# Performance work log

Hardware: AMD Instinct MI355X
Metric: run time of the kernel (lower is better)

The kernel has to match this reference:

```python
import jax, jax.numpy as jnp
import numpy as np

LP = 512   # paragraph length (sequential steps)
LQ = 512   # question/context length attended over
B = 24     # batch_size global in source
IN = 150   # in_size (encoder output dim)
H = 150    # self.hidden_size = 2*75


def setup_inputs() -> dict:
    key = jax.random.key(0)
    ks = jax.random.split(key, 12)
    sc = 1.0 / np.sqrt(2 * IN)  # keep pre-activations in a sane range
    return {
        "up": jax.random.normal(ks[0], (LP, B, IN), jnp.float32),
        "uq": jax.random.normal(ks[1], (LQ, B, IN), jnp.float32),
        "v0": jax.random.normal(ks[2], (B, H), jnp.float32),
        "V": jax.random.normal(ks[3], (B, H, 1), jnp.float32),
        "Wp": jax.random.normal(ks[4], (H, 2 * IN), jnp.float32) * sc,
        "Wq": jax.random.normal(ks[5], (H, 2 * IN), jnp.float32) * sc,
        "Wv": jax.random.normal(ks[6], (H, H), jnp.float32) * sc,
        "Wg": jax.random.normal(ks[7], (4 * IN, 4 * IN), jnp.float32) * sc,
        "w_ih": jax.random.normal(ks[8], (3 * H, 2 * IN), jnp.float32) * sc,
        "w_hh": jax.random.normal(ks[9], (3 * H, H), jnp.float32) * sc,
        "b_ih": jnp.zeros((3 * H,), jnp.float32),
        "b_hh": jnp.zeros((3 * H,), jnp.float32),
    }


def _gru_cell(x, h, w_ih, w_hh, b_ih, b_hh):
    # torch.nn.GRUCell semantics
    gi = x @ w_ih.T + b_ih            # [B, 3H]
    gh = h @ w_hh.T + b_hh            # [B, 3H]
    i_r, i_z, i_n = jnp.split(gi, 3, axis=1)
    h_r, h_z, h_n = jnp.split(gh, 3, axis=1)
    r = jax.nn.sigmoid(i_r + h_r)
    z = jax.nn.sigmoid(i_z + h_z)
    n = jnp.tanh(i_n + r * h_n)
    return (1.0 - z) * n + z * h


def reference(up, uq, v0, V, Wp, Wq, Wv, Wg, w_ih, w_hh, b_ih, b_hh):
    in_size = up.shape[-1]
    # mixer = arange -> up[mixer] == up, so concat duplicates features
    Up = jnp.concatenate([up, up], axis=-1)   # [lp, B, 2*in]
    Uq = jnp.concatenate([uq, uq], axis=-1)   # [lq, B, 2*in]
    WUq = jnp.einsum('lbd,hd->lbh', Uq, Wq)   # loop-invariant Wq(Uq), [lq,B,H]
    Uq_b = Uq.transpose(1, 0, 2)              # [B, lq, 2*in]
    Vv = V[:, :, 0]                            # [B, H]

    def step(v, Up_i):                         # Up_i: [B, 2*in]
        Wup = Up_i @ Wp.T                      # [B, H]
        Wvv = v @ Wv.T                         # [B, H]
        x = jnp.tanh(WUq + Wup[None] + Wvv[None])      # [lq, B, H]
        s = jnp.einsum('lbh,bh->bl', x, Vv)            # [B, lq]
        a = jax.nn.softmax(s, axis=1)                  # [B, lq]
        c = jnp.einsum('bl,bld->bd', a, Uq_b)          # [B, 2*in]
        r = jnp.concatenate([Up_i, c], axis=1)         # [B, 4*in]
        g = jax.nn.sigmoid(r @ Wg.T)                   # [B, 4*in]
        c_ = (g * r)[:, 2 * in_size:]                  # gated attended vector
        v_new = _gru_cell(c_, v, w_ih, w_hh, b_ih, b_hh)
        return v_new, v_new

    _, vs = jax.lax.scan(step, v0, Up)  # [lp, B, H]
    # nn.Dropout in eval mode = identity
    return vs
```

## Files before the change

### kernel.cpp

```cpp
#include <hip/hip_runtime.h>
#include <hip/hip_fp16.h>

typedef _Float16 h2 __attribute__((ext_vector_type(2)));

#define OFF_EW     0u
#define OFF_UQT    983040u
#define OFF_WAV    1904640u
#define OFF_WGC    1952640u
#define OFF_WIH    1976640u
#define OFF_WQST   2048640u
#define OFF_WPC    2071140u
#define OFF_WGU    2093940u
#define OFF_UPA    2139540u
#define OFF_GU     3982740u
#define OFF_FLAG   7669140u
#define WS_FLOATS  7669156u

__device__ __forceinline__ float fast_rcp(float x) { return __builtin_amdgcn_rcpf(x); }
__device__ __forceinline__ float fast_tanh(float x) {
  return 1.f - 2.f * fast_rcp(__expf(2.f * x) + 1.f);
}
__device__ __forceinline__ float fast_sigmoid(float x) {
  return fast_rcp(1.f + __expf(-x));
}

#if defined(__has_builtin)
#if __has_builtin(__builtin_amdgcn_fdot2)
#define HAVE_FDOT2 1
#endif
#if __has_builtin(__builtin_amdgcn_s_setprio)
#define HAVE_SETPRIO 1
#endif
#endif

__device__ __forceinline__ float fdot2(h2 a, h2 b, float c) {
#ifdef HAVE_FDOT2
  return __builtin_amdgcn_fdot2(a, b, c, false);
#else
  return c + (float)a[0] * (float)b[0] + (float)a[1] * (float)b[1];
#endif
}

__global__ void prep_weights(const float* __restrict__ Wq, const float* __restrict__ Wp,
                             const float* __restrict__ Wv, const float* __restrict__ Wg,
                             const float* __restrict__ w_ih, const float* __restrict__ w_hh,
                             float* __restrict__ ws) {
  float* wqsT = ws + OFF_WQST;
  float* WPC  = ws + OFF_WPC;
  float* WGU  = ws + OFF_WGU;
  _Float16* WAV = (_Float16*)(ws + OFF_WAV);
  _Float16* WGC = (_Float16*)(ws + OFF_WGC);
  _Float16* WIHh = (_Float16*)(ws + OFF_WIH);

  int idx = blockIdx.x * blockDim.x + threadIdx.x;
  int n = gridDim.x * blockDim.x;

  for (int i = idx; i < 150 * 150; i += n) {
    int d = i / 150, h = i - d * 150;
    wqsT[i] = Wq[h * 300 + d] + Wq[h * 300 + d + 150];
  }
  for (int i = idx; i < 600 * 160; i += n) {
    int r = i / 160, h = i - r * 160;
    float v = 0.f;
    if (h < 150) v = (r < 150) ? 2.f * Wv[r * 150 + h] : w_hh[(r - 150) * 150 + h];
    WAV[i] = (_Float16)v;
  }
  for (int i = idx; i < 300 * 160; i += n) {
    int r = i / 160, h = i - r * 160;
    int row = (300 + r) * 600;
    float v = (h < 150) ? Wg[row + 300 + h] + Wg[row + 450 + h] : 0.f;
    WGC[i] = (_Float16)v;
  }
  for (int i = idx; i < 450 * 320; i += n) {
    int r = i / 320, p = i - r * 320;
    float v = (p < 300) ? w_ih[r * 300 + p] : 0.f;
    WIHh[i] = (_Float16)v;
  }
  for (int i = idx; i < 150 * 152; i += n) {
    int h = i / 152, d = i - h * 152;
    WPC[i] = (d < 150) ? 2.f * (Wp[h * 300 + d] + Wp[h * 300 + 150 + d]) : 0.f;
  }
  for (int i = idx; i < 300 * 152; i += n) {
    int r = i / 152, d = i - r * 152;
    int row = (300 + r) * 600;
    WGU[i] = (d < 150) ? Wg[row + d] + Wg[row + 150 + d] : 0.f;
  }
}

__global__ __launch_bounds__(192) void prep_ew(const float* __restrict__ uq, float* __restrict__ ws) {
  const float* wqsT = ws + OFF_WQST;
  _Float16* EW = (_Float16*)(ws + OFF_EW);
  const int l = blockIdx.x, b = blockIdx.y;
  __shared__ float sx[150], sDot[150];
  const int t = threadIdx.x;
  if (t < 150) sx[t] = uq[((size_t)l * 24 + b) * 150 + t];
  __syncthreads();
  if (t < 150) {
    float acc = 0.f;
    for (int d = 0; d < 150; ++d) acc += sx[d] * wqsT[d * 150 + t];
    sDot[t] = acc;
  }
  __syncthreads();
  if (t < 160) {
    float val = 1.f;
    if (t < 150) {
      val = __expf(2.f * sDot[t]);
      val = fminf(fmaxf(val, 1e-7f), 60000.f);
    }
    EW[((size_t)b * 512 + l) * 160 + t] = (_Float16)val;
  }
}

__global__ void prep_uqt(const float* __restrict__ uq, float* __restrict__ ws) {
  _Float16* UQT = (_Float16*)(ws + OFF_UQT);
  int idx = blockIdx.x * blockDim.x + threadIdx.x;
  int n = gridDim.x * blockDim.x;
  for (int m = idx; m < 24 * 150 * 512; m += n) {
    int b = m / (150 * 512);
    int rem = m - b * 150 * 512;
    int r = rem >> 9;
    int l = rem & 511;
    UQT[m] = (_Float16)uq[((size_t)l * 24 + b) * 150 + r];
  }
}

__global__ __launch_bounds__(256) void prep_upagu(const float* __restrict__ up, float* __restrict__ ws) {
  const int b = blockIdx.x;
  const int it = blockIdx.y;
  __shared__ float sUp[64][153];
  for (int m = threadIdx.x; m < 64 * 150; m += 256) {
    int il = m / 150, d = m - il * 150;
    sUp[il][d] = up[(((size_t)(it * 64 + il)) * 24 + b) * 150 + d];
  }
  __syncthreads();
  const float* WGU = ws + OFF_WGU;
  const float* WPC = ws + OFF_WPC;
  float* GU  = ws + OFF_GU  + ((size_t)b * 512 + it * 64) * 300;
  float* UPA = ws + OFF_UPA + ((size_t)b * 512 + it * 64) * 150;
  const int il = threadIdx.x & 63, rl = threadIdx.x >> 6;
  for (int r = rl; r < 450; r += 4) {
    const float* w = (r < 300) ? (WGU + (size_t)r * 152) : (WPC + (size_t)(r - 300) * 152);
    float acc = 0.f;
    for (int d = 0; d < 150; ++d) acc = fmaf(w[d], sUp[il][d], acc);
    if (r < 300) GU[(size_t)il * 300 + r] = acc;
    else         UPA[(size_t)il * 150 + (r - 300)] = acc;
  }
}

__global__ __launch_bounds__(1024) void pq_main(
    const float* __restrict__ v0, const float* __restrict__ Vfull,
    const float* __restrict__ b_ih, const float* __restrict__ b_hh,
    float* __restrict__ ws, float* __restrict__ out) {
  const int blk = blockIdx.x;
  const int x = blk & 7, s = blk >> 3;
  const int t3 = (s == 0) ? 0 : (s == 10) ? 1 : (s == 20) ? 2 : -1;

  if (t3 < 0) {
    if (threadIdx.x >= 64) return;
    unsigned* flag = (unsigned*)(ws + OFF_FLAG);
    const unsigned long long start = __builtin_amdgcn_s_memrealtime();
    float a0 = 0.f, a1 = 0.f, a2 = 0.f, a3 = 0.f, a4 = 0.f, a5 = 0.f, a6 = 0.f, a7 = 0.f;
    const float m = 1.0000001f, c = 0.9999999f;
    for (;;) {
      #pragma unroll 32
      for (int k = 0; k < 1024; ++k) {
        a0 = fmaf(a0, m, c); a1 = fmaf(a1, m, c); a2 = fmaf(a2, m, c); a3 = fmaf(a3, m, c);
        a4 = fmaf(a4, m, c); a5 = fmaf(a5, m, c); a6 = fmaf(a6, m, c); a7 = fmaf(a7, m, c);
      }
      if (__hip_atomic_load(flag, __ATOMIC_RELAXED, __HIP_MEMORY_SCOPE_AGENT) == 0xDEADBEEFu) break;
      if (__builtin_amdgcn_s_memrealtime() - start > 3000000ull) break;
    }
    float sink = ((a0 + a1) + (a2 + a3)) + ((a4 + a5) + (a6 + a7));
    if (sink == 123.456789f) out[0] = sink;
    return;
  }

#ifdef HAVE_SETPRIO
  __builtin_amdgcn_s_setprio(3);
#endif

  const int b = x + 8 * t3;
  const int tid = threadIdx.x;

  const _Float16* EWh  = (const _Float16*)(ws + OFF_EW);
  const _Float16* UQTh = (const _Float16*)(ws + OFF_UQT);
  const _Float16* WAV  = (const _Float16*)(ws + OFF_WAV);
  const _Float16* WIHh = (const _Float16*)(ws + OFF_WIH);

  __shared__ float sTmpA[608];
  __shared__ float eyl[160];
  __shared__ float vvl[160];
  __shared__ float sS[512];
  __shared__ float sC[152];
  __shared__ float sGip[456], sBih[456], sBhh[456];
  __shared__ float sVl[152];
  __shared__ float sRed[8], sRedB[8];
  __shared__ float sSumV;
  __shared__ h2 sAhp2[272];
  __shared__ h2 vop2[80];
  __shared__ h2 ox2[80];
  __shared__ h2 cq2[160];
  __shared__ h2 sWv2[12000];
  __shared__ h2 sWGC2[24000];
  _Float16* sAhx = (_Float16*)sAhp2;
  _Float16* vop = (_Float16*)vop2;
  _Float16* ox  = (_Float16*)ox2;
  _Float16* cq  = (_Float16*)cq2;

  const int g = tid >> 3, j = tid & 7;
  const int g16 = tid >> 4, j16 = tid & 15;

  if (tid < 160) {
    vop[tid] = (_Float16)((tid < 150) ? v0[b * 150 + tid] : 0.f);
    vvl[tid] = (tid < 150) ? Vfull[b * 150 + tid] : 0.f;
    eyl[tid] = 1.f;
  } else if (tid < 320) {
    ox[tid - 160] = (_Float16)0.f;
  } else if (tid < 640) {
    cq[tid - 320] = (_Float16)0.f;
  }
  if (tid >= 512 && tid < 968) {
    int p = tid - 512;
    sBih[p] = (p < 450) ? b_ih[p] : 0.f;
    sBhh[p] = (p < 450) ? b_hh[p] : 0.f;
  }
  if (tid < 152) sVl[tid] = (tid < 150) ? v0[b * 150 + tid] : 0.f;
  {
    const unsigned* srcv = (const unsigned*)(ws + OFF_WAV);
    unsigned* dv = (unsigned*)sWv2;
    for (int k = tid; k < 12000; k += 1024) dv[k] = srcv[k];
    const unsigned* srcg = (const unsigned*)(ws + OFF_WGC);
    unsigned* dg = (unsigned*)sWGC2;
    for (int k = tid; k < 24000; k += 1024) dg[k] = srcg[k];
  }
  __syncthreads();
  if (tid >= 192 && tid < 256) {
    int ln = tid - 192;
    float sm = 0.f;
    for (int h = ln; h < 150; h += 64) sm += vvl[h];
    #pragma unroll
    for (int off = 32; off; off >>= 1) sm += __shfl_xor(sm, off, 64);
    if (ln == 0) sSumV = sm;
  }
  __syncthreads();

  for (int i = 0; i < 512; ++i) {
    {
      float ua0 = 0.f, ua1 = 0.f;
      if (j == 0) {
        const float* UPA = ws + OFF_UPA + ((size_t)b * 512 + i) * 150;
        ua0 = UPA[g];
        if (g < 22) ua1 = UPA[128 + g];
      }
      h2 va[10];
      #pragma unroll
      for (int t = 0; t < 10; ++t) va[t] = vop2[j * 10 + t];
      #pragma unroll
      for (int it = 0; it < 5; ++it) {
        const int r = g + (it << 7);
        if (r < 600) {
          h2 w[10];
          if (r < 150) {
            const h2* wp = sWv2 + r * 80 + j * 10;
            #pragma unroll
            for (int t = 0; t < 10; ++t) w[t] = wp[t];
          } else {
            const h2* wp = (const h2*)WAV + (size_t)r * 80 + j * 10;
            #pragma unroll
            for (int t = 0; t < 10; ++t) w[t] = wp[t];
          }
          float acc = 0.f;
          #pragma unroll
          for (int t = 0; t < 10; ++t) acc = fdot2(w[t], va[t], acc);
          acc += __shfl_xor(acc, 1, 64);
          acc += __shfl_xor(acc, 2, 64);
          acc += __shfl_xor(acc, 4, 64);
          if (j == 0) {
            if (r >= 150) sTmpA[r] = acc;
            else eyl[r] = fminf(__expf(((it == 0) ? ua0 : ua1) + acc), 1e30f);
          }
        }
      }
    }
    __syncthreads();
    {
      float ey[20], vv[20];
      #pragma unroll
      for (int t = 0; t < 20; ++t) { ey[t] = eyl[j * 20 + t]; vv[t] = vvl[j * 20 + t]; }
      #pragma unroll
      for (int it = 0; it < 4; ++it) {
        const int r = g + (it << 7);
        const h2* wp = (const h2*)(EWh + ((size_t)b * 512 + r) * 160) + j * 10;
        h2 w[10];
        #pragma unroll
        for (int t = 0; t < 10; ++t) w[t] = wp[t];
        float acc = 0.f;
        #pragma unroll
        for (int t = 0; t < 10; ++t) {
          float x1 = fmaf((float)w[t][0], ey[2 * t],     1.f);
          float y1 = fmaf((float)w[t][1], ey[2 * t + 1], 1.f);
          float num = fmaf(vv[2 * t], y1, vv[2 * t + 1] * x1);
          acc = fmaf(num, fast_rcp(x1 * y1), acc);
        }
        acc += __shfl_xor(acc, 1, 64);
        acc += __shfl_xor(acc, 2, 64);
        acc += __shfl_xor(acc, 4, 64);
        if (j == 0) sS[r] = sSumV - 2.f * acc;
      }
    }
    __syncthreads();
    {
      const bool act = tid < 512;
      float sv = act ? sS[tid] : -3.4e38f;
      float m = sv;
      #pragma unroll
      for (int off = 32; off; off >>= 1) m = fmaxf(m, __shfl_xor(m, off, 64));
      float e = act ? __expf(sv - m) : 0.f;
      float z = e;
      #pragma unroll
      for (int off = 32; off; off >>= 1) z += __shfl_xor(z, off, 64);
      if (act && (tid & 63) == 0) { sRed[tid >> 6] = m; sRedB[tid >> 6] = z; }
      __syncthreads();
      if (act) {
        float M = sRed[0];
        #pragma unroll
        for (int w = 1; w < 8; ++w) M = fmaxf(M, sRed[w]);
        float Z = 0.f;
        #pragma unroll
        for (int w = 0; w < 8; ++w) Z += sRedB[w] * __expf(sRed[w] - M);
        float a = (e * __expf(m - M)) * fast_rcp(Z);
        sAhx[(tid >> 5) * 34 + (tid & 31)] = (_Float16)a;
      }
    }
    __syncthreads();
    {
      h2 aa[16];
      #pragma unroll
      for (int t = 0; t < 16; ++t) aa[t] = sAhp2[j16 * 17 + t];
      #pragma unroll
      for (int it = 0; it < 3; ++it) {
        const int r = g16 + (it << 6);
        if (r < 150) {
          const h2* wp = (const h2*)(UQTh + ((size_t)b * 150 + r) * 512) + j16 * 16;
          h2 w[16];
          #pragma unroll
          for (int t = 0; t < 16; ++t) w[t] = wp[t];
          float acc = 0.f;
          #pragma unroll
          for (int t = 0; t < 16; ++t) acc = fdot2(aa[t], w[t], acc);
          acc += __shfl_xor(acc, 1, 64);
          acc += __shfl_xor(acc, 2, 64);
          acc += __shfl_xor(acc, 4, 64);
          acc += __shfl_xor(acc, 8, 64);
          if (j16 == 0) {
            sC[r] = acc;
            ox[r] = (_Float16)acc;
          }
        }
      }
    }
    __syncthreads();
    {
      float gu0 = 0.f, gu1 = 0.f, gu2 = 0.f;
      if (j == 0) {
        const float* GUp = ws + OFF_GU + ((size_t)b * 512 + i) * 300;
        gu0 = GUp[g];
        gu1 = GUp[128 + g];
        if (g < 44) gu2 = GUp[256 + g];
      }
      h2 xa[10];
      #pragma unroll
      for (int t = 0; t < 10; ++t) xa[t] = ox2[j * 10 + t];
      #pragma unroll
      for (int it = 0; it < 3; ++it) {
        const int r = g + (it << 7);
        if (r < 300) {
          const h2* wp = sWGC2 + r * 80 + j * 10;
          h2 w[10];
          #pragma unroll
          for (int t = 0; t < 10; ++t) w[t] = wp[t];
          float acc = 0.f;
          #pragma unroll
          for (int t = 0; t < 10; ++t) acc = fdot2(w[t], xa[t], acc);
          acc += __shfl_xor(acc, 1, 64);
          acc += __shfl_xor(acc, 2, 64);
          acc += __shfl_xor(acc, 4, 64);
          if (j == 0) {
            float gg = fast_sigmoid(acc + ((it == 0) ? gu0 : (it == 1) ? gu1 : gu2));
            int cj = (r >= 150) ? r - 150 : r;
            cq[r] = (_Float16)(gg * sC[cj]);
          }
        }
      }
    }
    __syncthreads();
    {
      h2 xa[20];
      #pragma unroll
      for (int t = 0; t < 20; ++t) xa[t] = cq2[j * 20 + t];
      #pragma unroll
      for (int it = 0; it < 4; ++it) {
        const int r = g + (it << 7);
        if (r < 450) {
          const h2* wp = (const h2*)WIHh + (size_t)r * 160 + j * 20;
          h2 w[20];
          #pragma unroll
          for (int t = 0; t < 20; ++t) w[t] = wp[t];
          float acc = 0.f;
          #pragma unroll
          for (int t = 0; t < 20; ++t) acc = fdot2(w[t], xa[t], acc);
          acc += __shfl_xor(acc, 1, 64);
          acc += __shfl_xor(acc, 2, 64);
          acc += __shfl_xor(acc, 4, 64);
          if (j == 0) sGip[r] = acc;
        }
      }
    }
    __syncthreads();
    if (tid < 150) {
      const int h = tid;
      float gh_r = sTmpA[150 + h] + sBhh[h];
      float gh_z = sTmpA[300 + h] + sBhh[150 + h];
      float gh_n = sTmpA[450 + h] + sBhh[300 + h];
      float rg = fast_sigmoid(sGip[h]       + sBih[h]       + gh_r);
      float zg = fast_sigmoid(sGip[150 + h] + sBih[150 + h] + gh_z);
      float nn = fast_tanh(sGip[300 + h] + sBih[300 + h] + rg * gh_n);
      float vn = (1.f - zg) * nn + zg * sVl[h];
      sVl[h] = vn;
      vop[h] = (_Float16)vn;
      out[((size_t)i * 24 + b) * 150 + h] = vn;
    }
    __syncthreads();
  }

  if (b == 0 && tid == 0) {
    __hip_atomic_store((unsigned*)(ws + OFF_FLAG), 0xDEADBEEFu,
                       __ATOMIC_RELAXED, __HIP_MEMORY_SCOPE_AGENT);
  }
}

extern "C" void kernel_launch(void* const* d_in, const int* in_sizes, int n_in,
                              void* d_out, int out_size, void* d_ws, size_t ws_size,
                              hipStream_t stream) {
  const float* up   = (const float*)d_in[0];
  const float* uq   = (const float*)d_in[1];
  const float* v0   = (const float*)d_in[2];
  const float* V    = (const float*)d_in[3];
  const float* Wp   = (const float*)d_in[4];
  const float* Wq   = (const float*)d_in[5];
  const float* Wv   = (const float*)d_in[6];
  const float* Wg   = (const float*)d_in[7];
  const float* w_ih = (const float*)d_in[8];
  const float* w_hh = (const float*)d_in[9];
  const float* b_ih = (const float*)d_in[10];
  const float* b_hh = (const float*)d_in[11];
  float* ws  = (float*)d_ws;
  float* out = (float*)d_out;

  if (ws_size < (size_t)WS_FLOATS * sizeof(float)) return;

  prep_weights<<<256, 256, 0, stream>>>(Wq, Wp, Wv, Wg, w_ih, w_hh, ws);
  prep_uqt<<<512, 256, 0, stream>>>(uq, ws);
  prep_ew<<<dim3(512, 24), 192, 0, stream>>>(uq, ws);
  prep_upagu<<<dim3(24, 8), 256, 0, stream>>>(up, ws);
  pq_main<<<256, 1024, 0, stream>>>(v0, V, b_ih, b_hh, ws, out);
}
```

Before: 6.792 ms.

## Split each batch's recurrence across two workgroups with global-memory flag exchange

Each batch element's sequential scan now runs on two workgroups instead of one. They split the v-projection columns, the attention score rows, the GRU input-gate rows and the hidden-unit update between them. Partial results go through a global scratch area, and two spin-wait flag handshakes per step join them. The aim is to halve the per-step matvec and weight-streaming work on the critical path. In exchange, each step pays two cross-CU synchronisations with atomic loads and stores, and the softmax and gating stages are still done redundantly by both workgroups.

```diff
diff --git a/kernel.cpp b/kernel.cpp
--- a/kernel.cpp
+++ b/kernel.cpp
@@ -14,7 +14,9 @@
 #define OFF_UPA    2139540u
 #define OFF_GU     3982740u
 #define OFF_FLAG   7669140u
-#define WS_FLOATS  7669156u
+#define OFF_EXG    7669156u
+#define OFF_XFLG   7718308u
+#define WS_FLOATS  7718708u
 
 __device__ __forceinline__ float fast_rcp(float x) { return __builtin_amdgcn_rcpf(x); }
 __device__ __forceinline__ float fast_tanh(float x) {
@@ -39,6 +41,13 @@
 #else
   return c + (float)a[0] * (float)b[0] + (float)a[1] * (float)b[1];
 #endif
+}
+
+__device__ __forceinline__ void ast(float* p, float v) {
+  __hip_atomic_store(p, v, __ATOMIC_RELAXED, __HIP_MEMORY_SCOPE_AGENT);
+}
+__device__ __forceinline__ float ald(const float* p) {
+  return __hip_atomic_load(p, __ATOMIC_RELAXED, __HIP_MEMORY_SCOPE_AGENT);
 }
 
 __global__ void prep_weights(const float* __restrict__ Wq, const float* __restrict__ Wp,
@@ -84,6 +93,10 @@
     int r = i / 152, d = i - r * 152;
     int row = (300 + r) * 600;
     WGU[i] = (d < 150) ? Wg[row + d] + Wg[row + 150 + d] : 0.f;
+  }
+  {
+    unsigned* xf = (unsigned*)(ws + OFF_XFLG);
+    for (int i = idx; i < 24 * 16; i += n) xf[i] = 0u;
   }
 }
 
@@ -153,7 +166,10 @@
     float* __restrict__ ws, float* __restrict__ out) {
   const int blk = blockIdx.x;
   const int x = blk & 7, s = blk >> 3;
-  const int t3 = (s == 0) ? 0 : (s == 10) ? 1 : (s == 20) ? 2 : -1;
+  int t3 = -1;
+  if (s == 0 || s == 1) t3 = 0;
+  else if (s == 10 || s == 11) t3 = 1;
+  else if (s == 20 || s == 21) t3 = 2;
 
   if (t3 < 0) {
     if (threadIdx.x >= 64) return;
@@ -179,20 +195,37 @@
   __builtin_amdgcn_s_setprio(3);
 #endif
 
+  const int hf = s & 1;
   const int b = x + 8 * t3;
   const int tid = threadIdx.x;
+
+  const int EYB = hf ? 80 : 0, EYW = hf ? 70 : 80;
+  const int SOFF2 = EYB >> 1;
+  const int NP4 = 3 * EYW;
 
   const _Float16* EWh  = (const _Float16*)(ws + OFF_EW);
   const _Float16* UQTh = (const _Float16*)(ws + OFF_UQT);
   const _Float16* WAV  = (const _Float16*)(ws + OFF_WAV);
   const _Float16* WIHh = (const _Float16*)(ws + OFF_WIH);
+  const float* UPAb = ws + OFF_UPA + (size_t)b * 512 * 150;
+  const float* GUb  = ws + OFF_GU  + (size_t)b * 512 * 300;
+
+  float* EX = ws + OFF_EXG + (size_t)b * 2048;
+  float* exP0 = EX;
+  float* exP1 = EX + 608;
+  float* exS  = EX + 1216;
+  float* exPmine = hf ? exP1 : exP0;
+  unsigned* FLG = (unsigned*)(ws + OFF_XFLG);
+  unsigned* myflag = FLG + (b * 16 + hf * 8);
+  unsigned* pflag  = FLG + (b * 16 + (1 - hf) * 8);
 
   __shared__ float sTmpA[608];
   __shared__ float eyl[160];
   __shared__ float vvl[160];
   __shared__ float sS[512];
   __shared__ float sC[152];
-  __shared__ float sGip[456], sBih[456], sBhh[456];
+  __shared__ float sGip[456];
+  __shared__ float sBih[456], sBhh[456];
   __shared__ float sVl[152];
   __shared__ float sRed[8], sRedB[8];
   __shared__ float sSumV;
@@ -244,43 +277,51 @@
   }
   __syncthreads();
 
+  #define XSYNC(K)                                                                   \
+    __syncthreads();                                                                 \
+    if (tid == 0) {                                                                  \
+      __hip_atomic_store(myflag + (K), (unsigned)(i + 1), __ATOMIC_RELAXED,          \
+                         __HIP_MEMORY_SCOPE_AGENT);                                  \
+      const unsigned long long t0 = __builtin_amdgcn_s_memrealtime();                \
+      while (__hip_atomic_load(pflag + (K), __ATOMIC_RELAXED,                        \
+                               __HIP_MEMORY_SCOPE_AGENT) < (unsigned)(i + 1)) {      \
+        __builtin_amdgcn_s_sleep(1);                                                 \
+        if (__builtin_amdgcn_s_memrealtime() - t0 > 20000000ull) break;     \
+      }                                                                              \
+    }                                                                                \
+    __syncthreads();
+
   for (int i = 0; i < 512; ++i) {
     {
-      float ua0 = 0.f, ua1 = 0.f;
-      if (j == 0) {
-        const float* UPA = ws + OFF_UPA + ((size_t)b * 512 + i) * 150;
-        ua0 = UPA[g];
-        if (g < 22) ua1 = UPA[128 + g];
-      }
-      h2 va[10];
-      #pragma unroll
-      for (int t = 0; t < 10; ++t) va[t] = vop2[j * 10 + t];
+      h2 va[5];
+      #pragma unroll
+      for (int t = 0; t < 5; ++t) va[t] = vop2[SOFF2 + j * 5 + t];
       #pragma unroll
       for (int it = 0; it < 5; ++it) {
         const int r = g + (it << 7);
         if (r < 600) {
-          h2 w[10];
-          if (r < 150) {
-            const h2* wp = sWv2 + r * 80 + j * 10;
-            #pragma unroll
-            for (int t = 0; t < 10; ++t) w[t] = wp[t];
-          } else {
-            const h2* wp = (const h2*)WAV + (size_t)r * 80 + j * 10;
-            #pragma unroll
-            for (int t = 0; t < 10; ++t) w[t] = wp[t];
-          }
+          const h2* wp = (r < 150) ? (sWv2 + r * 80 + SOFF2 + j * 5)
+                                   : ((const h2*)WAV + (size_t)r * 80 + SOFF2 + j * 5);
+          h2 w[5];
+          #pragma unroll
+          for (int t = 0; t < 5; ++t) w[t] = wp[t];
           float acc = 0.f;
           #pragma unroll
-          for (int t = 0; t < 10; ++t) acc = fdot2(w[t], va[t], acc);
+          for (int t = 0; t < 5; ++t) acc = fdot2(w[t], va[t], acc);
           acc += __shfl_xor(acc, 1, 64);
           acc += __shfl_xor(acc, 2, 64);
           acc += __shfl_xor(acc, 4, 64);
-          if (j == 0) {
-            if (r >= 150) sTmpA[r] = acc;
-            else eyl[r] = fminf(__expf(((it == 0) ? ua0 : ua1) + acc), 1e30f);
-          }
+          if (j == 0) ast(&exPmine[r], acc);
         }
       }
+    }
+    XSYNC(0)
+    if (tid < 150) {
+      float p = ald(&exP0[tid]) + ald(&exP1[tid]);
+      eyl[tid] = fminf(__expf(UPAb[(size_t)i * 150 + tid] + p), 1e30f);
+    } else if (tid >= 512 && tid < 962) {
+      const int r = tid - 362;
+      sTmpA[r] = ald(&exP0[r]) + ald(&exP1[r]);
     }
     __syncthreads();
     {
@@ -288,9 +329,9 @@
       #pragma unroll
       for (int t = 0; t < 20; ++t) { ey[t] = eyl[j * 20 + t]; vv[t] = vvl[j * 20 + t]; }
       #pragma unroll
-      for (int it = 0; it < 4; ++it) {
-        const int r = g + (it << 7);
-        const h2* wp = (const h2*)(EWh + ((size_t)b * 512 + r) * 160) + j * 10;
+      for (int it = 0; it < 2; ++it) {
+        const int l = 256 * hf + g + (it << 7);
+        const h2* wp = (const h2*)(EWh + ((size_t)b * 512 + l) * 160) + j * 10;
         h2 w[10];
         #pragma unroll
         for (int t = 0; t < 10; ++t) w[t] = wp[t];
@@ -305,13 +346,18 @@
         acc += __shfl_xor(acc, 1, 64);
         acc += __shfl_xor(acc, 2, 64);
         acc += __shfl_xor(acc, 4, 64);
-        if (j == 0) sS[r] = sSumV - 2.f * acc;
-      }
-    }
-    __syncthreads();
+        if (j == 0) {
+          float sval = sSumV - 2.f * acc;
+          sS[l] = sval;
+          ast(&exS[l], sval);
+        }
+      }
+    }
+    XSYNC(1)
     {
       const bool act = tid < 512;
-      float sv = act ? sS[tid] : -3.4e38f;
+      float sv = -3.4e38f;
+      if (act) sv = ((tid >> 8) == hf) ? sS[tid] : ald(&exS[tid]);
       float m = sv;
       #pragma unroll
       for (int off = 32; off; off >>= 1) m = fmaxf(m, __shfl_xor(m, off, 64));
@@ -363,7 +409,7 @@
     {
       float gu0 = 0.f, gu1 = 0.f, gu2 = 0.f;
       if (j == 0) {
-        const float* GUp = ws + OFF_GU + ((size_t)b * 512 + i) * 300;
+        const float* GUp = GUb + (size_t)i * 300;
         gu0 = GUp[g];
         gu1 = GUp[128 + g];
         if (g < 44) gu2 = GUp[256 + g];
@@ -399,9 +445,12 @@
       #pragma unroll
       for (int t = 0; t < 20; ++t) xa[t] = cq2[j * 20 + t];
       #pragma unroll
-      for (int it = 0; it < 4; ++it) {
-        const int r = g + (it << 7);
-        if (r < 450) {
+      for (int it = 0; it < 2; ++it) {
+        const int idx = g + (it << 7);
+        if (idx < NP4) {
+          const int k = (idx >= 2 * EYW) ? 2 : (idx >= EYW) ? 1 : 0;
+          const int o = idx - k * EYW;
+          const int r = k * 150 + EYB + o;
           const h2* wp = (const h2*)WIHh + (size_t)r * 160 + j * 20;
           h2 w[20];
           #pragma unroll
@@ -417,8 +466,8 @@
       }
     }
     __syncthreads();
-    if (tid < 150) {
-      const int h = tid;
+    if (tid < EYW) {
+      const int h = EYB + tid;
       float gh_r = sTmpA[150 + h] + sBhh[h];
       float gh_z = sTmpA[300 + h] + sBhh[150 + h];
       float gh_n = sTmpA[450 + h] + sBhh[300 + h];
@@ -433,10 +482,11 @@
     __syncthreads();
   }
 
-  if (b == 0 && tid == 0) {
+  if (b == 0 && hf == 0 && tid == 0) {
     __hip_atomic_store((unsigned*)(ws + OFF_FLAG), 0xDEADBEEFu,
                        __ATOMIC_RELAXED, __HIP_MEMORY_SCOPE_AGENT);
   }
+  #undef XSYNC
 }
 
 extern "C" void kernel_launch(void* const* d_in, const int* in_sizes, int n_in,
```

After: 6.369 ms. 6.2% less time.
